# Kernel optimization log

Measured on AMD Instinct MI355X. Metric: run time of the kernel, lower is better.

The kernel has to match this reference:

```python
import jax, jax.numpy as jnp
import numpy as np

N = 100000
E = 1600000
NEG_SLOPE = 0.2

def _gat_layer(x, src, dst, W, a_s, a_d, b, n):
    # GATConv (heads=1): h = xW; alpha_ij = softmax_i(leaky_relu(a_s.h_j + a_d.h_i))
    h = x @ W                                   # [N, F]
    s_src = h @ a_s                             # [N]
    s_dst = h @ a_d                             # [N]
    logits = jax.nn.leaky_relu(s_src[src] + s_dst[dst], NEG_SLOPE)  # [E]
    m = jax.ops.segment_max(logits, dst, num_segments=n)
    m = jnp.where(jnp.isfinite(m), m, 0.0)
    w = jnp.exp(logits - m[dst])
    denom = jax.ops.segment_sum(w, dst, num_segments=n)
    alpha = w / (denom[dst] + 1e-16)            # neighbor softmax per target node
    out = jax.ops.segment_sum(alpha[:, None] * h[src], dst, num_segments=n)
    return out + b

def setup_inputs() -> dict:
    key = jax.random.key(0)
    ks = jax.random.split(key, 12)
    def glorot(k, shape):
        fan = shape[0] + shape[-1] if len(shape) > 1 else shape[0]
        return jax.random.normal(k, shape, jnp.float32) * jnp.sqrt(2.0 / fan)
    x = jax.random.normal(ks[0], (N, 128), jnp.float32)
    edge_index = jax.random.randint(ks[1], (2, E), 0, N, dtype=jnp.int32)
    return {
        'x': x, 'edge_index': edge_index,
        'W1': glorot(ks[2], (128, 64)), 'a1s': glorot(ks[3], (64,)), 'a1d': glorot(ks[4], (64,)), 'b1': jnp.zeros((64,), jnp.float32),
        'W2': glorot(ks[5], (64, 64)), 'a2s': glorot(ks[6], (64,)), 'a2d': glorot(ks[7], (64,)), 'b2': jnp.zeros((64,), jnp.float32),
        'W3': glorot(ks[8], (64, 32)), 'a3s': glorot(ks[9], (32,)), 'a3d': glorot(ks[10], (32,)), 'b3': jnp.zeros((32,), jnp.float32),
    }

def reference(x, edge_index, W1, a1s, a1d, b1, W2, a2s, a2d, b2, W3, a3s, a3d, b3):
    n = x.shape[0]
    # PyG GATConv adds self-loops by default
    loops = jnp.arange(n, dtype=edge_index.dtype)
    src = jnp.concatenate([edge_index[0], loops])
    dst = jnp.concatenate([edge_index[1], loops])
    h = _gat_layer(x, src, dst, W1, a1s, a1d, b1, n)
    h = jax.nn.relu(h)  # dropout is identity in eval mode
    h = _gat_layer(h, src, dst, W2, a2s, a2d, b2, n)
    h = jax.nn.relu(h)
    h = _gat_layer(h, src, dst, W3, a3s, a3d, b3, n)
    return jax.nn.log_softmax(h, axis=1)
```

## Files before the change

### kernel.cpp

```cpp
#include <hip/hip_runtime.h>
#include <hip/hip_fp16.h>
#include <cstddef>
#include <cstdint>

#define NEG_SLOPE 0.2f

__device__ __forceinline__ unsigned short f2bf(float f) {
    unsigned int u = __float_as_uint(f);
    u = (u + 0x7fff + ((u >> 16) & 1)) >> 16;
    return (unsigned short)u;
}
__device__ __forceinline__ float bf_lo(unsigned int u) { return __uint_as_float(u << 16); }
__device__ __forceinline__ float bf_hi(unsigned int u) { return __uint_as_float(u & 0xffff0000u); }

typedef __attribute__((ext_vector_type(8))) short bf16x8;
typedef __attribute__((ext_vector_type(4))) float f32x4;


constexpr int SCAN_TILE = 1024;

__global__ __launch_bounds__(256) void scan_pass1(const int* __restrict__ in,
                                                  int* __restrict__ bsum, int n) {
    const int tid = threadIdx.x;
    const int base = blockIdx.x * SCAN_TILE + tid * 4;
    int s = 0;
#pragma unroll
    for (int k = 0; k < 4; ++k) {
        int i = base + k;
        if (i < n) s += in[i];
    }
    for (int o = 1; o < 64; o <<= 1) s += __shfl_xor(s, o);
    __shared__ int wsum[4];
    if ((tid & 63) == 0) wsum[tid >> 6] = s;
    __syncthreads();
    if (tid == 0) bsum[blockIdx.x] = wsum[0] + wsum[1] + wsum[2] + wsum[3];
}

__global__ __launch_bounds__(256) void scan_pass2(int* __restrict__ bsum,
                                                  int* __restrict__ out,
                                                  int nb, int n) {
    __shared__ int sh[1024];
    const int tid = threadIdx.x;
    for (int i = tid; i < nb; i += 256) sh[i] = bsum[i];
    __syncthreads();
    if (tid == 0) {
        int run = 0;
        for (int i = 0; i < nb; ++i) { int c = sh[i]; sh[i] = run; run += c; }
        out[n] = run;
    }
    __syncthreads();
    for (int i = tid; i < nb; i += 256) bsum[i] = sh[i];
}

__global__ __launch_bounds__(256) void scan_pass3(const int* __restrict__ in,
                                                  const int* __restrict__ bsum,
                                                  int* __restrict__ out, int n) {
    const int tid = threadIdx.x;
    const int lane = tid & 63;
    const int wid = tid >> 6;
    const int base = blockIdx.x * SCAN_TILE + tid * 4;
    int v[4];
    int tsum = 0;
#pragma unroll
    for (int k = 0; k < 4; ++k) {
        int i = base + k;
        v[k] = (i < n) ? in[i] : 0;
        tsum += v[k];
    }
    int inc = tsum;
    for (int o = 1; o < 64; o <<= 1) {
        int t = __shfl_up(inc, o);
        if (lane >= o) inc += t;
    }
    __shared__ int wtot[4];
    if (lane == 63) wtot[wid] = inc;
    __syncthreads();
    int woff = 0;
    for (int w = 0; w < wid; ++w) woff += wtot[w];
    int off = bsum[blockIdx.x] + woff + (inc - tsum);
#pragma unroll
    for (int k = 0; k < 4; ++k) {
        int i = base + k;
        if (i < n) { out[i] = off; off += v[k]; }
    }
}


constexpr int BIN_BLOCKS = 256;
constexpr int MAX_NBK = 1024;

__global__ __launch_bounds__(256) void bin_hist_k(const int* __restrict__ dst, int E,
                                                  int* __restrict__ cntb, int nbk,
                                                  int chunk) {
    __shared__ int hist[MAX_NBK];
    for (int i = threadIdx.x; i < nbk; i += 256) hist[i] = 0;
    __syncthreads();
    const int lo = blockIdx.x * chunk;
    const int hi = min(lo + chunk, E);
    for (int e = lo + threadIdx.x; e < hi; e += 256)
        atomicAdd(&hist[dst[e] >> 7], 1);
    __syncthreads();
    for (int i = threadIdx.x; i < nbk; i += 256)
        cntb[i * gridDim.x + blockIdx.x] = hist[i];
}

__global__ __launch_bounds__(256) void bin_scatter_k(const int* __restrict__ ei, int E,
                                                     const int* __restrict__ obb,
                                                     int* __restrict__ eb, int nbk,
                                                     int chunk) {
    __shared__ int cur[MAX_NBK];
    __shared__ int off_s[MAX_NBK];
    const int B = gridDim.x;
    for (int i = threadIdx.x; i < nbk; i += 256) {
        cur[i] = 0;
        off_s[i] = obb[i * B + blockIdx.x];
    }
    __syncthreads();
    const int lo = blockIdx.x * chunk;
    const int hi = min(lo + chunk, E);
    for (int e = lo + threadIdx.x; e < hi; e += 256) {
        int s = ei[e];
        int d = ei[E + e];
        int b = d >> 7;
        int idx = atomicAdd(&cur[b], 1);
        eb[off_s[b] + idx] = (s << 7) | (d & 127);
    }
}

__global__ __launch_bounds__(256) void bucket_cnt_k(const int* __restrict__ eb,
                                                    const int* __restrict__ obb,
                                                    int* __restrict__ cnt,
                                                    int B, int n) {
    __shared__ int c[128];
    const int b = blockIdx.x;
    const int t = threadIdx.x;
    const int beg = obb[b * B];
    const int end = obb[(b + 1) * B];
    if (t < 128) c[t] = 1;
    __syncthreads();
    for (int i = beg + t; i < end; i += 256)
        atomicAdd(&c[eb[i] & 127], 1);
    __syncthreads();
    const int node = b * 128 + t;
    if (t < 128 && node < n) cnt[node] = c[t];
}

__global__ __launch_bounds__(256) void bucket_scatter_k(const int* __restrict__ eb,
                                                        const int* __restrict__ obb,
                                                        const int* __restrict__ row_ptr,
                                                        int* __restrict__ col,
                                                        int B, int n) {
    __shared__ int c[128];
    __shared__ int rp[128];
    const int b = blockIdx.x;
    const int t = threadIdx.x;
    const int beg = obb[b * B];
    const int end = obb[(b + 1) * B];
    const int node = b * 128 + t;
    if (t < 128) {
        c[t] = 1;
        if (node < n) {
            rp[t] = row_ptr[node];
            col[rp[t]] = node;
        }
    }
    __syncthreads();
    for (int i = beg + t; i < end; i += 256) {
        int p = eb[i];
        int dl = p & 127;
        int idx = atomicAdd(&c[dl], 1);
        col[rp[dl] + idx] = p >> 7;
    }
}


template <int K, int F>
__launch_bounds__(256)
__global__ void gemm_mfma_k(const float* __restrict__ x, const float* __restrict__ W,
                            const float* __restrict__ a_s, const float* __restrict__ a_d,
                            unsigned short* __restrict__ hb, float* __restrict__ ss,
                            float* __restrict__ sd, int n) {
    constexpr int MT = 64;
    constexpr int KP = K + 8;
    constexpr int NT = F / 16;
    constexpr int KC = K / 32;

    __shared__ unsigned short xb[MT * KP];
    __shared__ unsigned short wb[F * KP];

    const int tid = threadIdx.x;
    const int lane = tid & 63;
    const int wv = tid >> 6;
    const int base = blockIdx.x * MT;

    for (int i = tid; i < MT * K / 4; i += 256) {
        int row = i / (K / 4);
        int c4 = i % (K / 4);
        float4 v = make_float4(0.f, 0.f, 0.f, 0.f);
        if (base + row < n)
            v = *(const float4*)&x[(size_t)(base + row) * K + 4 * c4];
        ushort4 b;
        b.x = f2bf(v.x); b.y = f2bf(v.y); b.z = f2bf(v.z); b.w = f2bf(v.w);
        *(ushort4*)&xb[row * KP + 4 * c4] = b;
    }
    for (int i = tid; i < K * F / 4; i += 256) {
        int k = i / (F / 4);
        int n4 = i % (F / 4);
        float4 v = *(const float4*)&W[(size_t)k * F + 4 * n4];
        wb[(4 * n4 + 0) * KP + k] = f2bf(v.x);
        wb[(4 * n4 + 1) * KP + k] = f2bf(v.y);
        wb[(4 * n4 + 2) * KP + k] = f2bf(v.z);
        wb[(4 * n4 + 3) * KP + k] = f2bf(v.w);
    }
    __syncthreads();

    const int mrow = lane & 15;
    const int quad = lane >> 4;

    f32x4 acc[NT];
#pragma unroll
    for (int t = 0; t < NT; ++t) acc[t] = (f32x4){0.f, 0.f, 0.f, 0.f};

#pragma unroll
    for (int kc = 0; kc < KC; ++kc) {
        const int kof = kc * 32 + quad * 8;
        bf16x8 af = *(const bf16x8*)&xb[(wv * 16 + mrow) * KP + kof];
#pragma unroll
        for (int t = 0; t < NT; ++t) {
            bf16x8 bf = *(const bf16x8*)&wb[(t * 16 + mrow) * KP + kof];
            acc[t] = __builtin_amdgcn_mfma_f32_16x16x32_bf16(af, bf, acc[t], 0, 0, 0);
        }
    }

    float as_c[NT], ad_c[NT];
#pragma unroll
    for (int t = 0; t < NT; ++t) { as_c[t] = a_s[t * 16 + mrow]; ad_c[t] = a_d[t * 16 + mrow]; }

#pragma unroll
    for (int r = 0; r < 4; ++r) {
        const int node = base + wv * 16 + quad * 4 + r;
        float ps = 0.f, pd = 0.f;
#pragma unroll
        for (int t = 0; t < NT; ++t) {
            ps = fmaf(acc[t][r], as_c[t], ps);
            pd = fmaf(acc[t][r], ad_c[t], pd);
        }
#pragma unroll
        for (int o = 1; o < 16; o <<= 1) {
            ps += __shfl_xor(ps, o);
            pd += __shfl_xor(pd, o);
        }
        if (node < n) {
#pragma unroll
            for (int t = 0; t < NT; ++t)
                hb[(size_t)node * F + t * 16 + mrow] = f2bf(acc[t][r]);
            if (mrow == 0) { ss[node] = ps; sd[node] = pd; }
        }
    }
}


template <int F, int S, bool RELU, bool LOGSM>
__launch_bounds__(256)
__global__ void gat_agg_k(const int* __restrict__ row_ptr, const int* __restrict__ col,
                          const unsigned short* __restrict__ hb,
                          const float* __restrict__ ss, const float* __restrict__ sd,
                          const float* __restrict__ bias,
                          float* __restrict__ out, int n) {
    constexpr int NPW = 64 / S;
    constexpr int NL = F / 8;
    constexpr int Q = S / NL;
    const int lane = threadIdx.x & 63;
    const int ls   = lane % S;
    const int q    = ls / NL;
    const int cl   = ls % NL;
    const int lbase = lane - ls;
    const int wave = (blockIdx.x * blockDim.x + threadIdx.x) >> 6;
    const int node = wave * NPW + lane / S;
    if (node >= n) return;

    const int beg = row_ptr[node];
    const int end = row_ptr[node + 1];
    const float sdv = sd[node];

    float m = -__builtin_inff();
    float s = 0.f;
    float acc[8];
#pragma unroll
    for (int i = 0; i < 8; ++i) acc[i] = 0.f;

    for (int base = beg; base < end; base += S) {
        const int j = base + ls;
        int   c = 0;
        float logit = -__builtin_inff();
        if (j < end) {
            c = col[j];
            float z = ss[c] + sdv;
            logit = (z > 0.f) ? z : NEG_SLOPE * z;
        }
        float cm = logit;
#pragma unroll
        for (int o = S / 2; o; o >>= 1) cm = fmaxf(cm, __shfl_xor(cm, o));
        const float newm = fmaxf(m, cm);
        const float scale = __expf(m - newm);
        s *= scale;
#pragma unroll
        for (int i = 0; i < 8; ++i) acc[i] *= scale;
        const float w = __expf(logit - newm);
        float wsum = w;
#pragma unroll
        for (int o = S / 2; o; o >>= 1) wsum += __shfl_xor(wsum, o);
        s += wsum;
        m = newm;

        const unsigned int pk =
            ((unsigned int)__half_as_ushort(__float2half(w)) << 17) | (unsigned int)c;

        const int cnt = min(S, end - base);
        for (int t = 0; Q * t < cnt; ++t) {
            const int e = Q * t + q;
            const unsigned int pe = __shfl(pk, lbase + e);
            const int   ct = (int)(pe & 0x1ffffu);
            const float wt = __half2float(__ushort_as_half((unsigned short)(pe >> 17)));
            const uint4 hv = *(const uint4*)&hb[(size_t)ct * F + 8 * cl];
            acc[0] = fmaf(wt, bf_lo(hv.x), acc[0]);
            acc[1] = fmaf(wt, bf_hi(hv.x), acc[1]);
            acc[2] = fmaf(wt, bf_lo(hv.y), acc[2]);
            acc[3] = fmaf(wt, bf_hi(hv.y), acc[3]);
            acc[4] = fmaf(wt, bf_lo(hv.z), acc[4]);
            acc[5] = fmaf(wt, bf_hi(hv.z), acc[5]);
            acc[6] = fmaf(wt, bf_lo(hv.w), acc[6]);
            acc[7] = fmaf(wt, bf_hi(hv.w), acc[7]);
        }
    }

#pragma unroll
    for (int o = NL; o < S; o <<= 1) {
#pragma unroll
        for (int i = 0; i < 8; ++i) acc[i] += __shfl_xor(acc[i], o);
    }

    const float inv = 1.f / (s + 1e-16f);
    float val[8];
#pragma unroll
    for (int i = 0; i < 8; ++i) {
        val[i] = acc[i] * inv + bias[8 * cl + i];
        if (RELU) val[i] = fmaxf(val[i], 0.f);
    }
    if (LOGSM) {
        float lm = val[0];
#pragma unroll
        for (int i = 1; i < 8; ++i) lm = fmaxf(lm, val[i]);
#pragma unroll
        for (int o = 1; o < NL; o <<= 1) lm = fmaxf(lm, __shfl_xor(lm, o));
        float ex = 0.f;
#pragma unroll
        for (int i = 0; i < 8; ++i) ex += __expf(val[i] - lm);
#pragma unroll
        for (int o = 1; o < NL; o <<= 1) ex += __shfl_xor(ex, o);
        const float lse = lm + __logf(ex);
#pragma unroll
        for (int i = 0; i < 8; ++i) val[i] -= lse;
    }
    if (q == 0) {
        float4 v0 = make_float4(val[0], val[1], val[2], val[3]);
        float4 v1 = make_float4(val[4], val[5], val[6], val[7]);
        *(float4*)&out[(size_t)node * F + 8 * cl] = v0;
        *(float4*)&out[(size_t)node * F + 8 * cl + 4] = v1;
    }
}


extern "C" void kernel_launch(void* const* d_in, const int* in_sizes, int n_in,
                              void* d_out, int out_size, void* d_ws, size_t ws_size,
                              hipStream_t stream) {
    const float* x  = (const float*)d_in[0];
    const int*   ei = (const int*)d_in[1];
    const float* W1 = (const float*)d_in[2];
    const float* a1s = (const float*)d_in[3];
    const float* a1d = (const float*)d_in[4];
    const float* b1  = (const float*)d_in[5];
    const float* W2 = (const float*)d_in[6];
    const float* a2s = (const float*)d_in[7];
    const float* a2d = (const float*)d_in[8];
    const float* b2  = (const float*)d_in[9];
    const float* W3 = (const float*)d_in[10];
    const float* a3s = (const float*)d_in[11];
    const float* a3d = (const float*)d_in[12];
    const float* b3  = (const float*)d_in[13];

    const int N = in_sizes[0] / 128;
    const int E = in_sizes[1] / 2;
    const int NBK = (N + 127) / 128;
    const int B = BIN_BLOCKS;

    char* wp = (char*)d_ws;
    auto alloc = [&](size_t bytes) -> void* {
        void* p = wp;
        wp += (bytes + 255) & ~(size_t)255;
        return p;
    };
    int* cnt     = (int*)alloc((size_t)N * 4);
    int* row_ptr = (int*)alloc((size_t)(N + 1) * 4);
    int* col     = (int*)alloc((size_t)(E + N) * 4);
    unsigned short* hb = (unsigned short*)alloc((size_t)N * 64 * 2);
    float* ss  = (float*)alloc((size_t)N * 4);
    float* sd  = (float*)alloc((size_t)N * 4);
    float* o1  = (float*)alloc((size_t)N * 64 * 4);
    float* o2  = (float*)alloc((size_t)N * 64 * 4);
    int* cntb  = (int*)alloc((size_t)NBK * B * 4);
    int* obb   = (int*)alloc(((size_t)NBK * B + 1) * 4);
    int* bsum  = (int*)alloc(1024 * 4);
    int* eb = (int*)o2;

    const int chunk = (E + B - 1) / B;
    const int nb2 = (NBK * B + SCAN_TILE - 1) / SCAN_TILE;
    const int nbn = (N + SCAN_TILE - 1) / SCAN_TILE;

    bin_hist_k<<<B, 256, 0, stream>>>(ei + E, E, cntb, NBK, chunk);
    scan_pass1<<<nb2, 256, 0, stream>>>(cntb, bsum, NBK * B);
    scan_pass2<<<1, 256, 0, stream>>>(bsum, obb, nb2, NBK * B);
    scan_pass3<<<nb2, 256, 0, stream>>>(cntb, bsum, obb, NBK * B);
    bin_scatter_k<<<B, 256, 0, stream>>>(ei, E, obb, eb, NBK, chunk);
    bucket_cnt_k<<<NBK, 256, 0, stream>>>(eb, obb, cnt, B, N);
    scan_pass1<<<nbn, 256, 0, stream>>>(cnt, bsum, N);
    scan_pass2<<<1, 256, 0, stream>>>(bsum, row_ptr, nbn, N);
    scan_pass3<<<nbn, 256, 0, stream>>>(cnt, bsum, row_ptr, N);
    bucket_scatter_k<<<NBK, 256, 0, stream>>>(eb, obb, row_ptr, col, B, N);

    const int GB = (N + 63) / 64;

    gemm_mfma_k<128, 64><<<GB, 256, 0, stream>>>(x, W1, a1s, a1d, hb, ss, sd, N);
    gat_agg_k<64, 32, true, false><<<(N + 7) / 8, 256, 0, stream>>>(row_ptr, col, hb, ss, sd, b1, o1, N);

    gemm_mfma_k<64, 64><<<GB, 256, 0, stream>>>(o1, W2, a2s, a2d, hb, ss, sd, N);
    gat_agg_k<64, 32, true, false><<<(N + 7) / 8, 256, 0, stream>>>(row_ptr, col, hb, ss, sd, b2, o2, N);

    gemm_mfma_k<64, 32><<<GB, 256, 0, stream>>>(o2, W3, a3s, a3d, hb, ss, sd, N);
    gat_agg_k<32, 16, false, true><<<(N + 15) / 16, 256, 0, stream>>>(row_ptr, col, hb, ss, sd, b3,
                                                                      (float*)d_out, N);
}
```

Baseline: 325.8 us.

## Fuse CSR bucket count, scan, and scatter into one kernel; unroll aggregation loop

Merges bucket counting, the node-level prefix scan (three scan launches) and the column scatter into a single per-bucket kernel. Each bucket derives its row_ptr base from the bin offsets plus the self-loop count and does a local wave scan, which removes four kernel launches and the cnt buffer round trip. The aggregation inner loop is also unrolled by two so two neighbour gathers can be in flight at once, at the cost of more registers.

```diff
diff --git a/kernel.cpp b/kernel.cpp
--- a/kernel.cpp
+++ b/kernel.cpp
@@ -127,43 +127,44 @@
     }
 }
 
-__global__ __launch_bounds__(256) void bucket_cnt_k(const int* __restrict__ eb,
-                                                    const int* __restrict__ obb,
-                                                    int* __restrict__ cnt,
-                                                    int B, int n) {
-    __shared__ int c[128];
-    const int b = blockIdx.x;
-    const int t = threadIdx.x;
-    const int beg = obb[b * B];
-    const int end = obb[(b + 1) * B];
-    if (t < 128) c[t] = 1;
-    __syncthreads();
-    for (int i = beg + t; i < end; i += 256)
-        atomicAdd(&c[eb[i] & 127], 1);
-    __syncthreads();
-    const int node = b * 128 + t;
-    if (t < 128 && node < n) cnt[node] = c[t];
-}
-
-__global__ __launch_bounds__(256) void bucket_scatter_k(const int* __restrict__ eb,
-                                                        const int* __restrict__ obb,
-                                                        const int* __restrict__ row_ptr,
-                                                        int* __restrict__ col,
-                                                        int B, int n) {
+__global__ __launch_bounds__(256) void bucket_build_k(const int* __restrict__ eb,
+                                                      const int* __restrict__ obb,
+                                                      int* __restrict__ row_ptr,
+                                                      int* __restrict__ col,
+                                                      int B, int n, int nbk) {
     __shared__ int c[128];
     __shared__ int rp[128];
     const int b = blockIdx.x;
     const int t = threadIdx.x;
     const int beg = obb[b * B];
     const int end = obb[(b + 1) * B];
+    const int bbase = beg + b * 128;
+    if (t < 128) c[t] = 1;
+    __syncthreads();
+    for (int i = beg + t; i < end; i += 256)
+        atomicAdd(&c[eb[i] & 127], 1);
+    __syncthreads();
+    if (t < 64) {
+        int v0 = c[2 * t], v1 = c[2 * t + 1];
+        int pair = v0 + v1;
+        int inc = pair;
+        for (int o = 1; o < 64; o <<= 1) {
+            int u = __shfl_up(inc, o);
+            if (t >= o) inc += u;
+        }
+        int ex = inc - pair;
+        rp[2 * t] = bbase + ex;
+        rp[2 * t + 1] = bbase + ex + v0;
+    }
+    __syncthreads();
     const int node = b * 128 + t;
-    if (t < 128) {
-        c[t] = 1;
-        if (node < n) {
-            rp[t] = row_ptr[node];
-            col[rp[t]] = node;
-        }
-    }
+    if (t < 128 && node < n) {
+        row_ptr[node] = rp[t];
+        col[rp[t]] = node;
+    }
+    if (b == 0 && t == 0) row_ptr[n] = obb[nbk * B] + n;
+    __syncthreads();
+    if (t < 128) c[t] = 1;
     __syncthreads();
     for (int i = beg + t; i < end; i += 256) {
         int p = eb[i];
@@ -317,12 +318,35 @@
             ((unsigned int)__half_as_ushort(__float2half(w)) << 17) | (unsigned int)c;
 
         const int cnt = min(S, end - base);
-        for (int t = 0; Q * t < cnt; ++t) {
-            const int e = Q * t + q;
-            const unsigned int pe = __shfl(pk, lbase + e);
-            const int   ct = (int)(pe & 0x1ffffu);
+        int t = 0;
+        for (; Q * (t + 1) < cnt; t += 2) {
+            const unsigned int pe0 = __shfl(pk, lbase + Q * t + q);
+            const unsigned int pe1 = __shfl(pk, lbase + Q * (t + 1) + q);
+            const uint4 hv0 = *(const uint4*)&hb[(size_t)(pe0 & 0x1ffffu) * F + 8 * cl];
+            const uint4 hv1 = *(const uint4*)&hb[(size_t)(pe1 & 0x1ffffu) * F + 8 * cl];
+            const float wt0 = __half2float(__ushort_as_half((unsigned short)(pe0 >> 17)));
+            const float wt1 = __half2float(__ushort_as_half((unsigned short)(pe1 >> 17)));
+            acc[0] = fmaf(wt0, bf_lo(hv0.x), acc[0]);
+            acc[1] = fmaf(wt0, bf_hi(hv0.x), acc[1]);
+            acc[2] = fmaf(wt0, bf_lo(hv0.y), acc[2]);
+            acc[3] = fmaf(wt0, bf_hi(hv0.y), acc[3]);
+            acc[4] = fmaf(wt0, bf_lo(hv0.z), acc[4]);
+            acc[5] = fmaf(wt0, bf_hi(hv0.z), acc[5]);
+            acc[6] = fmaf(wt0, bf_lo(hv0.w), acc[6]);
+            acc[7] = fmaf(wt0, bf_hi(hv0.w), acc[7]);
+            acc[0] = fmaf(wt1, bf_lo(hv1.x), acc[0]);
+            acc[1] = fmaf(wt1, bf_hi(hv1.x), acc[1]);
+            acc[2] = fmaf(wt1, bf_lo(hv1.y), acc[2]);
+            acc[3] = fmaf(wt1, bf_hi(hv1.y), acc[3]);
+            acc[4] = fmaf(wt1, bf_lo(hv1.z), acc[4]);
+            acc[5] = fmaf(wt1, bf_hi(hv1.z), acc[5]);
+            acc[6] = fmaf(wt1, bf_lo(hv1.w), acc[6]);
+            acc[7] = fmaf(wt1, bf_hi(hv1.w), acc[7]);
+        }
+        if (Q * t < cnt) {
+            const unsigned int pe = __shfl(pk, lbase + Q * t + q);
+            const uint4 hv = *(const uint4*)&hb[(size_t)(pe & 0x1ffffu) * F + 8 * cl];
             const float wt = __half2float(__ushort_as_half((unsigned short)(pe >> 17)));
-            const uint4 hv = *(const uint4*)&hb[(size_t)ct * F + 8 * cl];
             acc[0] = fmaf(wt, bf_lo(hv.x), acc[0]);
             acc[1] = fmaf(wt, bf_hi(hv.x), acc[1]);
             acc[2] = fmaf(wt, bf_lo(hv.y), acc[2]);
@@ -400,7 +424,6 @@
         wp += (bytes + 255) & ~(size_t)255;
         return p;
     };
-    int* cnt     = (int*)alloc((size_t)N * 4);
     int* row_ptr = (int*)alloc((size_t)(N + 1) * 4);
     int* col     = (int*)alloc((size_t)(E + N) * 4);
     unsigned short* hb = (unsigned short*)alloc((size_t)N * 64 * 2);
@@ -415,18 +438,13 @@
 
     const int chunk = (E + B - 1) / B;
     const int nb2 = (NBK * B + SCAN_TILE - 1) / SCAN_TILE;
-    const int nbn = (N + SCAN_TILE - 1) / SCAN_TILE;
 
     bin_hist_k<<<B, 256, 0, stream>>>(ei + E, E, cntb, NBK, chunk);
     scan_pass1<<<nb2, 256, 0, stream>>>(cntb, bsum, NBK * B);
     scan_pass2<<<1, 256, 0, stream>>>(bsum, obb, nb2, NBK * B);
     scan_pass3<<<nb2, 256, 0, stream>>>(cntb, bsum, obb, NBK * B);
     bin_scatter_k<<<B, 256, 0, stream>>>(ei, E, obb, eb, NBK, chunk);
-    bucket_cnt_k<<<NBK, 256, 0, stream>>>(eb, obb, cnt, B, N);
-    scan_pass1<<<nbn, 256, 0, stream>>>(cnt, bsum, N);
-    scan_pass2<<<1, 256, 0, stream>>>(bsum, row_ptr, nbn, N);
-    scan_pass3<<<nbn, 256, 0, stream>>>(cnt, bsum, row_ptr, N);
-    bucket_scatter_k<<<NBK, 256, 0, stream>>>(eb, obb, row_ptr, col, B, N);
+    bucket_build_k<<<NBK, 256, 0, stream>>>(eb, obb, row_ptr, col, B, N, NBK);
 
     const int GB = (N + 63) / 64;
 
```

Result: faster. 307.8 us (-5.5%).
